# Performance work log

Hardware: AMD Instinct MI355X
Metric: run time of the kernel (lower is better)

Reference implementation:

```python
import jax, jax.numpy as jnp
import numpy as np

B, SEQ, PRED, DM = 16, 2048, 2048, 64
P = SEQ + PRED            # PointNum = 4096, per-node feature length
NLAYER, HID = 3, 4096     # MLPNums, ggdmodel hidden sizes
NH, HS = 16, 4096         # NumAttentionHeads, HiddenSize
G_CONST, K = 1.0, 8
NN = DM * DM              # 4096 == P, MHSA input dim (required by original code)


def setup_inputs() -> dict:
    key = jax.random.key(0)
    ks = jax.random.split(key, 11)
    s_mlp = 1.0 / np.sqrt(P).astype(np.float32)
    s_att = 1.0 / np.sqrt(NN).astype(np.float32)
    s_out = 1.0 / np.sqrt(HS).astype(np.float32)
    return {
        "x": jax.random.normal(ks[0], (B, P, DM), jnp.float32),
        "W_mlp": jax.random.normal(ks[1], (NLAYER, P, HID), jnp.float32) * s_mlp,
        "b_mlp": jnp.zeros((NLAYER, HID), jnp.float32),
        "Wq": jax.random.normal(ks[2], (NN, HS), jnp.float32) * s_att,
        "bq": jnp.zeros((HS,), jnp.float32),
        "Wk": jax.random.normal(ks[3], (NN, HS), jnp.float32) * s_att,
        "bk": jnp.zeros((HS,), jnp.float32),
        "Wv": jax.random.normal(ks[4], (NN, HS), jnp.float32) * s_att,
        "bv": jnp.zeros((HS,), jnp.float32),
        "Wo": jax.random.normal(ks[5], (HS, HS), jnp.float32) * s_out,
        "bo": jnp.zeros((HS,), jnp.float32),
    }


def _grav_adj(h):
    # h: [B, N, D] node features -> symmetrized, top-K masked gravity adjacency [B, N, N]
    norm = jnp.linalg.norm(h, axis=-1)                      # [B, N]
    m = jnp.sum(h, axis=-1) / norm                          # node "mass"
    sim = jnp.einsum('bnd,bmd->bnm', h, h) / (norm[:, :, None] * norm[:, None, :])
    F = G_CONST * m[:, :, None] * m[:, None, :] * sim * sim  # gravity matrix
    kth = jax.lax.top_k(F, K)[0][..., -1:]                  # per-row Kth largest value
    F = jnp.where(F >= kth, F, 0.0)                         # keep only top-K per row
    F = jnp.maximum(F, 0.0)                                 # ReLU
    return 0.5 * (F + jnp.swapaxes(F, -1, -2))              # symmetrize


def reference(x, W_mlp, b_mlp, Wq, bq, Wk, bk, Wv, bv, Wo, bo):
    h = jnp.swapaxes(x, 1, 2)                               # [B, N=DM, P]
    adjs = [_grav_adj(h)]
    for l in range(NLAYER):                                 # each MLP applied to the same h
        hv = h @ W_mlp[l] + b_mlp[l]                        # [B, N, HID]
        adjs.append(_grav_adj(hv))
    A = jnp.stack(adjs, axis=1)                             # [B, L, N, N], L = NLAYER + 1
    Lseq = A.shape[1]
    tok = A.reshape(B, Lseq, NN)                            # L tokens of dim N*N
    dh = HS // NH
    q = (tok @ Wq + bq).reshape(B, Lseq, NH, dh)
    k = (tok @ Wk + bk).reshape(B, Lseq, NH, dh)
    v = (tok @ Wv + bv).reshape(B, Lseq, NH, dh)
    scores = jnp.einsum('blhd,bmhd->bhlm', q, k) / np.sqrt(dh).astype(np.float32)
    attn = jax.nn.softmax(scores, axis=-1)
    ctx = jnp.einsum('bhlm,bmhd->blhd', attn, v).reshape(B, Lseq, HS)
    out = ctx @ Wo + bo                                     # [B, L, HS]
    return jnp.where(out > 0.5, out, 0.0)
```

## Files before the change

kernel.cpp:

```cpp
#include <hip/hip_runtime.h>
#include <math.h>


#define B16 16
#define PDIM 4096
#define NNODE 64
#define NCHUNK 32
#define KCG 128

typedef __attribute__((ext_vector_type(8))) short bf16x8;
typedef __attribute__((ext_vector_type(4))) float f32x4;
typedef __attribute__((ext_vector_type(4))) unsigned short us4;
typedef __attribute__((ext_vector_type(8))) unsigned short us8;

__device__ inline void split2(float x, unsigned short& h, unsigned short& l) {
  unsigned u = __float_as_uint(x);
  unsigned hu = (u + 0x7fffu + ((u >> 16) & 1u)) & 0xffff0000u;
  h = (unsigned short)(hu >> 16);
  float lo = x - __uint_as_float(hu);
  unsigned u2 = __float_as_uint(lo);
  l = (unsigned short)((u2 + 0x7fffu + ((u2 >> 16) & 1u)) >> 16);
}

__device__ inline void gload16(const void* g, void* lds) {
  __builtin_amdgcn_global_load_lds((const unsigned int*)g, (unsigned int*)lds, 16, 0, 0);
}

__global__ __launch_bounds__(256) void k_transpose(const float* __restrict__ x,
                                                   float* __restrict__ h,
                                                   unsigned short* __restrict__ AhT,
                                                   unsigned short* __restrict__ AlT,
                                                   int mode) {
  __shared__ float t[64][65];
  int b = blockIdx.y;
  int p0 = blockIdx.x * 64;
  const float* xb = x + (size_t)b * PDIM * NNODE;
#pragma unroll
  for (int i = 0; i < 16; ++i) {
    int e = i * 256 + threadIdx.x;
    int p = e >> 6, n = e & 63;
    t[p][n] = xb[(size_t)p0 * 64 + e];
  }
  __syncthreads();
  if (mode != 2) {
    float* hb = h + (size_t)b * NNODE * PDIM;
#pragma unroll
    for (int i = 0; i < 16; ++i) {
      int e = i * 256 + threadIdx.x;
      int n = e >> 6, p = e & 63;
      hb[(size_t)n * PDIM + p0 + p] = t[p][n];
    }
  }
  if (mode == 0) return;
#pragma unroll
  for (int j = 0; j < 2; ++j) {
    int cid = j * 256 + threadIdx.x;
    int n2 = cid >> 3, kg8 = cid & 7;
    us8 hv_, lv_;
#pragma unroll
    for (int e = 0; e < 8; ++e) {
      unsigned short hh, ll;
      split2(t[kg8 * 8 + e][n2], hh, ll);
      hv_[e] = hh; lv_[e] = ll;
    }
    int m = b * 64 + n2;
    int ks = (p0 >> 5) + (kg8 >> 2);
    size_t idx = (((size_t)(m >> 7) * 128 + ks) * 8 + ((m >> 4) & 7)) * 512 +
                 (size_t)((n2 & 15) + 16 * (kg8 & 3)) * 8;
    *(us8*)&AhT[idx] = hv_;
    *(us8*)&AlT[idx] = lv_;
  }
}

__global__ __launch_bounds__(256) void k_wsplit(const float* __restrict__ W,
                                                unsigned short* __restrict__ WhT,
                                                unsigned short* __restrict__ WlT) {
  __shared__ float Wt[32][132];
  int nb = blockIdx.x, kb = blockIdx.y;
  int tid = threadIdx.x;
#pragma unroll
  for (int i = 0; i < 4; ++i) {
    int idx = i * 256 + tid;
    int row = idx >> 5, c4 = idx & 31;
    float4 v = *(const float4*)&W[(size_t)(kb * 32 + row) * 4096 + nb * 128 + c4 * 4];
    *(float4*)&Wt[row][c4 * 4] = v;
  }
  __syncthreads();
#pragma unroll
  for (int j = 0; j < 2; ++j) {
    int cid = j * 256 + tid;
    int nl = cid & 127, kg = cid >> 7;
    us8 hv_, lv_;
#pragma unroll
    for (int e = 0; e < 8; ++e) {
      unsigned short hh, ll;
      split2(Wt[kg * 8 + e][nl], hh, ll);
      hv_[e] = hh; lv_[e] = ll;
    }
    size_t idx = (((size_t)nb * 128 + kb) * 8 + (nl >> 4)) * 512 +
                 (size_t)((nl & 15) + 16 * kg) * 8;
    *(us8*)&WhT[idx] = hv_;
    *(us8*)&WlT[idx] = lv_;
  }
}

__global__ __launch_bounds__(512) void k_gemm_bf16(
    const unsigned short* __restrict__ Ah, const unsigned short* __restrict__ Al,
    const unsigned short* __restrict__ Bh, const unsigned short* __restrict__ Bl,
    float* __restrict__ Cp, int Ksteps, int ksplit, int N, int mstore) {
  __shared__ unsigned short sAh[2][4096], sAl[2][4096];
  __shared__ unsigned short sBh[2][4096], sBl[2][4096];
  int tid = threadIdx.x;
  int l = tid & 63, wid = tid >> 6;
  int wr = wid >> 2, wc = wid & 3;
  int nb = blockIdx.x, mb = blockIdx.y, z = blockIdx.z;
  int spp = Ksteps / ksplit;
  int ks0 = z * spp;

  const size_t abase = ((size_t)mb * Ksteps + ks0) * 4096 + tid * 8;
  const size_t bbase = ((size_t)nb * Ksteps + ks0) * 4096 + tid * 8;

  f32x4 acc[4][2];
#pragma unroll
  for (int i = 0; i < 4; ++i)
#pragma unroll
    for (int j = 0; j < 2; ++j) acc[i][j] = (f32x4){0.f, 0.f, 0.f, 0.f};

  gload16(Ah + abase, &sAh[0][tid * 8]);
  gload16(Al + abase, &sAl[0][tid * 8]);
  gload16(Bh + bbase, &sBh[0][tid * 8]);
  gload16(Bl + bbase, &sBl[0][tid * 8]);
  gload16(Ah + abase + 4096, &sAh[1][tid * 8]);
  gload16(Al + abase + 4096, &sAl[1][tid * 8]);
  gload16(Bh + bbase + 4096, &sBh[1][tid * 8]);
  gload16(Bl + bbase + 4096, &sBl[1][tid * 8]);

  for (int t = 0; t < spp; ++t) {
    int buf = t & 1;
    if (t + 1 < spp) asm volatile("s_waitcnt vmcnt(4)" ::: "memory");
    else             asm volatile("s_waitcnt vmcnt(0)" ::: "memory");
    __builtin_amdgcn_s_barrier();
    asm volatile("" ::: "memory");

    bf16x8 ah[4], al4[4], bh2[2], bl2[2];
#pragma unroll
    for (int mt = 0; mt < 4; ++mt) {
      ah[mt]  = *(const bf16x8*)&sAh[buf][(wr * 4 + mt) * 512 + l * 8];
      al4[mt] = *(const bf16x8*)&sAl[buf][(wr * 4 + mt) * 512 + l * 8];
    }
#pragma unroll
    for (int nt = 0; nt < 2; ++nt) {
      bh2[nt] = *(const bf16x8*)&sBh[buf][(wc * 2 + nt) * 512 + l * 8];
      bl2[nt] = *(const bf16x8*)&sBl[buf][(wc * 2 + nt) * 512 + l * 8];
    }
#pragma unroll
    for (int mt = 0; mt < 4; ++mt)
#pragma unroll
      for (int nt = 0; nt < 2; ++nt) {
        acc[mt][nt] = __builtin_amdgcn_mfma_f32_16x16x32_bf16(ah[mt],  bh2[nt], acc[mt][nt], 0, 0, 0);
        acc[mt][nt] = __builtin_amdgcn_mfma_f32_16x16x32_bf16(ah[mt],  bl2[nt], acc[mt][nt], 0, 0, 0);
        acc[mt][nt] = __builtin_amdgcn_mfma_f32_16x16x32_bf16(al4[mt], bh2[nt], acc[mt][nt], 0, 0, 0);
      }

    asm volatile("" ::: "memory");
    __builtin_amdgcn_s_barrier();
    asm volatile("" ::: "memory");
    if (t + 2 < spp) {
      size_t off = (size_t)(t + 2) * 4096;
      gload16(Ah + abase + off, &sAh[buf][tid * 8]);
      gload16(Al + abase + off, &sAl[buf][tid * 8]);
      gload16(Bh + bbase + off, &sBh[buf][tid * 8]);
      gload16(Bl + bbase + off, &sBl[buf][tid * 8]);
    }
  }

  int n0 = nb * 128, m0 = mb * 128;
  float* Cz = Cp + (size_t)z * mstore * N;
#pragma unroll
  for (int mt = 0; mt < 4; ++mt)
#pragma unroll
    for (int nt = 0; nt < 2; ++nt) {
      int col = n0 + wc * 32 + nt * 16 + (l & 15);
#pragma unroll
      for (int r = 0; r < 4; ++r) {
        int row = m0 + wr * 64 + mt * 16 + ((l >> 4) << 2) + r;
        if (row < mstore) Cz[(size_t)row * N + col] = acc[mt][nt][r];
      }
    }
}

__global__ __launch_bounds__(512) void k_gemm_wsf32(
    const unsigned short* __restrict__ Ah, const unsigned short* __restrict__ Al,
    const float* __restrict__ W0, const float* __restrict__ W1,
    const float* __restrict__ W2, float* __restrict__ Cp, int ksplit) {
  __shared__ unsigned short sAh[2][2048], sAl[2][2048];
  __shared__ unsigned short sBh[2][4096], sBl[2][4096];
  int tid = threadIdx.x;
  int l = tid & 63, wid = tid >> 6;
  int wr = wid >> 2, wc = wid & 3;
  int nb = blockIdx.x, z = blockIdx.z;
  int mat = z / ksplit, kz = z - mat * ksplit;
  const float* W = (mat == 0) ? W0 : ((mat == 1) ? W1 : W2);
  int nsteps = 128 / ksplit;
  int ks0 = kz * nsteps;
  int n0 = nb * 128;

  const float* wbase = W + (size_t)((l >> 4) * 8) * 4096 + n0 + wid * 16 + (l & 15);
  int sidx = wid * 512 + l * 8;

  f32x4 acc[2][2];
#pragma unroll
  for (int i = 0; i < 2; ++i)
#pragma unroll
    for (int j = 0; j < 2; ++j) acc[i][j] = (f32x4){0.f, 0.f, 0.f, 0.f};

  {
    if (tid < 256) gload16(Ah + (size_t)ks0 * 4096 + tid * 8, &sAh[0][tid * 8]);
    else           gload16(Al + (size_t)ks0 * 4096 + (tid - 256) * 8, &sAl[0][(tid - 256) * 8]);
    float wv[8];
#pragma unroll
    for (int e = 0; e < 8; ++e) wv[e] = wbase[(size_t)ks0 * 131072 + (size_t)e * 4096];
    us8 hi, lo;
#pragma unroll
    for (int e = 0; e < 8; ++e) {
      unsigned short hh, ll;
      split2(wv[e], hh, ll);
      hi[e] = hh; lo[e] = ll;
    }
    *(us8*)&sBh[0][sidx] = hi;
    *(us8*)&sBl[0][sidx] = lo;
  }
  __syncthreads();

  int buf = 0;
  for (int t = 0; t < nsteps; ++t) {
    bool more = (t + 1 < nsteps);
    float wv[8];
    if (more) {
      int ks = ks0 + t + 1;
      if (tid < 256) gload16(Ah + (size_t)ks * 4096 + tid * 8, &sAh[buf ^ 1][tid * 8]);
      else           gload16(Al + (size_t)ks * 4096 + (tid - 256) * 8, &sAl[buf ^ 1][(tid - 256) * 8]);
#pragma unroll
      for (int e = 0; e < 8; ++e) wv[e] = wbase[(size_t)ks * 131072 + (size_t)e * 4096];
    }
    bf16x8 aH[2], aL[2], bH[2], bL[2];
#pragma unroll
    for (int i = 0; i < 2; ++i) {
      aH[i] = *(const bf16x8*)&sAh[buf][(wr * 2 + i) * 512 + l * 8];
      aL[i] = *(const bf16x8*)&sAl[buf][(wr * 2 + i) * 512 + l * 8];
      bH[i] = *(const bf16x8*)&sBh[buf][(wc * 2 + i) * 512 + l * 8];
      bL[i] = *(const bf16x8*)&sBl[buf][(wc * 2 + i) * 512 + l * 8];
    }
#pragma unroll
    for (int i = 0; i < 2; ++i)
#pragma unroll
      for (int j = 0; j < 2; ++j) {
        acc[i][j] = __builtin_amdgcn_mfma_f32_16x16x32_bf16(aH[i], bH[j], acc[i][j], 0, 0, 0);
        acc[i][j] = __builtin_amdgcn_mfma_f32_16x16x32_bf16(aH[i], bL[j], acc[i][j], 0, 0, 0);
        acc[i][j] = __builtin_amdgcn_mfma_f32_16x16x32_bf16(aL[i], bH[j], acc[i][j], 0, 0, 0);
      }
    if (more) {
      us8 hi, lo;
#pragma unroll
      for (int e = 0; e < 8; ++e) {
        unsigned short hh, ll;
        split2(wv[e], hh, ll);
        hi[e] = hh; lo[e] = ll;
      }
      *(us8*)&sBh[buf ^ 1][sidx] = hi;
      *(us8*)&sBl[buf ^ 1][sidx] = lo;
    }
    __syncthreads();
    buf ^= 1;
  }

  float* Cz = Cp + (size_t)z * 262144;
#pragma unroll
  for (int i = 0; i < 2; ++i)
#pragma unroll
    for (int j = 0; j < 2; ++j) {
      int col = n0 + wc * 32 + j * 16 + (l & 15);
#pragma unroll
      for (int r = 0; r < 4; ++r) {
        int row = (wr * 2 + i) * 16 + ((l >> 4) << 2) + r;
        Cz[(size_t)row * 4096 + col] = acc[i][j][r];
      }
    }
}

__global__ __launch_bounds__(256) void k_gram_fuse(
    const float* __restrict__ Cp, const float* __restrict__ bias,
    float* __restrict__ Gp, float* __restrict__ Sp, int nparts) {
  __shared__ unsigned short sZh[2048], sZl[2048];
  int zk = blockIdx.x, b = blockIdx.y;
  int tid = threadIdx.x;
  int l = tid & 63, w = tid >> 6;
  int srow = tid >> 2, skq = tid & 3;
  const float* cbase = Cp + (size_t)(b * 64 + srow) * 4096;
  int swidx = (srow >> 4) * 512 + (skq * 16 + (srow & 15)) * 8;

  f32x4 acc[4], racc;
#pragma unroll
  for (int j = 0; j < 4; ++j) acc[j] = (f32x4){0.f, 0.f, 0.f, 0.f};
  racc = (f32x4){0.f, 0.f, 0.f, 0.f};
  bf16x8 ones;
#pragma unroll
  for (int e = 0; e < 8; ++e) ones[e] = (short)0x3F80;

  for (int s = 0; s < 4; ++s) {
    int k0 = zk * 128 + s * 32 + skq * 8;
    float v[8];
#pragma unroll
    for (int e = 0; e < 8; ++e) v[e] = bias[k0 + e];
    for (int p = 0; p < nparts; ++p) {
      const float* pp = cbase + (size_t)p * 4194304 + k0;
      float4 a0 = *(const float4*)pp;
      float4 a1 = *(const float4*)(pp + 4);
      v[0] += a0.x; v[1] += a0.y; v[2] += a0.z; v[3] += a0.w;
      v[4] += a1.x; v[5] += a1.y; v[6] += a1.z; v[7] += a1.w;
    }
    us8 hi, lo;
#pragma unroll
    for (int e = 0; e < 8; ++e) {
      unsigned short hh, ll;
      split2(v[e], hh, ll);
      hi[e] = hh; lo[e] = ll;
    }
    *(us8*)&sZh[swidx] = hi;
    *(us8*)&sZl[swidx] = lo;
    __syncthreads();
    bf16x8 bh[4], bl4[4];
#pragma unroll
    for (int nt = 0; nt < 4; ++nt) {
      bh[nt]  = *(const bf16x8*)&sZh[nt * 512 + l * 8];
      bl4[nt] = *(const bf16x8*)&sZl[nt * 512 + l * 8];
    }
    bf16x8 ah = bh[w], al = bl4[w];
#pragma unroll
    for (int nt = 0; nt < 4; ++nt) {
      acc[nt] = __builtin_amdgcn_mfma_f32_16x16x32_bf16(ah, bh[nt], acc[nt], 0, 0, 0);
      acc[nt] = __builtin_amdgcn_mfma_f32_16x16x32_bf16(ah, bl4[nt], acc[nt], 0, 0, 0);
      acc[nt] = __builtin_amdgcn_mfma_f32_16x16x32_bf16(al, bh[nt], acc[nt], 0, 0, 0);
    }
    racc = __builtin_amdgcn_mfma_f32_16x16x32_bf16(ah, ones, racc, 0, 0, 0);
    racc = __builtin_amdgcn_mfma_f32_16x16x32_bf16(al, ones, racc, 0, 0, 0);
    __syncthreads();
  }

  float* Gz = Gp + ((size_t)zk * B16 + b) * 4096;
#pragma unroll
  for (int nt = 0; nt < 4; ++nt) {
    int col = nt * 16 + (l & 15);
#pragma unroll
    for (int r = 0; r < 4; ++r) {
      int row = w * 16 + ((l >> 4) << 2) + r;
      Gz[row * 64 + col] = acc[nt][r];
    }
  }
  if ((l & 15) == 0) {
    float* Sz = Sp + ((size_t)zk * B16 + b) * 64;
#pragma unroll
    for (int r = 0; r < 4; ++r) Sz[w * 16 + ((l >> 4) << 2) + r] = racc[r];
  }
}

__global__ __launch_bounds__(256) void k_gram_mfma(
    const unsigned short* __restrict__ Zh, const unsigned short* __restrict__ Zl,
    float* __restrict__ Gp, float* __restrict__ Sp,
    int bs1, int ks_stride, int nsteps) {
  __shared__ unsigned short sZh[2][2048], sZl[2][2048];
  int z = blockIdx.x, b = blockIdx.y;
  int tid = threadIdx.x;
  int l = tid & 63, w = tid >> 6;
  size_t zbase = (size_t)(b >> 1) * 524288 + (size_t)(b & 1) * bs1;
  int ks0 = z * nsteps;

  f32x4 acc[4], racc;
#pragma unroll
  for (int j = 0; j < 4; ++j) acc[j] = (f32x4){0.f, 0.f, 0.f, 0.f};
  racc = (f32x4){0.f, 0.f, 0.f, 0.f};
  bf16x8 ones;
#pragma unroll
  for (int e = 0; e < 8; ++e) ones[e] = (short)0x3F80;

  gload16(Zh + zbase + (size_t)ks0 * ks_stride + tid * 8, &sZh[0][tid * 8]);
  gload16(Zl + zbase + (size_t)ks0 * ks_stride + tid * 8, &sZl[0][tid * 8]);
  __syncthreads();

  int buf = 0;
  for (int t = 0; t < nsteps; ++t) {
    if (t + 1 < nsteps) {
      size_t off = zbase + (size_t)(ks0 + t + 1) * ks_stride + tid * 8;
      gload16(Zh + off, &sZh[buf ^ 1][tid * 8]);
      gload16(Zl + off, &sZl[buf ^ 1][tid * 8]);
    }
    bf16x8 bh[4], bl4[4];
#pragma unroll
    for (int nt = 0; nt < 4; ++nt) {
      bh[nt]  = *(const bf16x8*)&sZh[buf][nt * 512 + l * 8];
      bl4[nt] = *(const bf16x8*)&sZl[buf][nt * 512 + l * 8];
    }
    bf16x8 ah = bh[w], al = bl4[w];
#pragma unroll
    for (int nt = 0; nt < 4; ++nt) {
      acc[nt] = __builtin_amdgcn_mfma_f32_16x16x32_bf16(ah, bh[nt], acc[nt], 0, 0, 0);
      acc[nt] = __builtin_amdgcn_mfma_f32_16x16x32_bf16(ah, bl4[nt], acc[nt], 0, 0, 0);
      acc[nt] = __builtin_amdgcn_mfma_f32_16x16x32_bf16(al, bh[nt], acc[nt], 0, 0, 0);
    }
    racc = __builtin_amdgcn_mfma_f32_16x16x32_bf16(ah, ones, racc, 0, 0, 0);
    racc = __builtin_amdgcn_mfma_f32_16x16x32_bf16(al, ones, racc, 0, 0, 0);
    __syncthreads();
    buf ^= 1;
  }

  float* Gz = Gp + ((size_t)z * B16 + b) * 4096;
#pragma unroll
  for (int nt = 0; nt < 4; ++nt) {
    int col = nt * 16 + (l & 15);
#pragma unroll
    for (int r = 0; r < 4; ++r) {
      int row = w * 16 + ((l >> 4) << 2) + r;
      Gz[row * 64 + col] = acc[nt][r];
    }
  }
  if ((l & 15) == 0) {
    float* Sz = Sp + ((size_t)z * B16 + b) * 64;
#pragma unroll
    for (int r = 0; r < 4; ++r) Sz[w * 16 + ((l >> 4) << 2) + r] = racc[r];
  }
}

__global__ __launch_bounds__(256) void k_gred(const float* __restrict__ Gp,
                                              const float* __restrict__ Sp,
                                              float* __restrict__ G,
                                              float* __restrict__ S, int slot, int nc) {
  int idx = blockIdx.x * 256 + threadIdx.x;
  if (idx < 65536) {
    float s = 0.f;
    for (int c = 0; c < nc; ++c) s += Gp[(size_t)c * 65536 + idx];
    G[(size_t)slot * 65536 + idx] = s;
  } else if (idx < 66560) {
    int i2 = idx - 65536;
    float s = 0.f;
    for (int c = 0; c < nc; ++c) s += Sp[(size_t)c * 1024 + i2];
    S[(size_t)slot * 1024 + i2] = s;
  }
}

__global__ __launch_bounds__(256) void k_redqkv(const float* __restrict__ Cp,
                                                const float* __restrict__ bq,
                                                const float* __restrict__ bk,
                                                const float* __restrict__ bv,
                                                float* __restrict__ q,
                                                float* __restrict__ k,
                                                float* __restrict__ v) {
  int idx = blockIdx.x * 256 + threadIdx.x;
  int mat = idx >> 18;
  int rn = idx & ((1 << 18) - 1);
  int n = rn & 4095;
  const float* base = Cp + (size_t)mat * 16 * 262144;
  float s = 0.f;
#pragma unroll
  for (int p = 0; p < 16; ++p) s += base[(size_t)p * 262144 + rn];
  if (mat == 0) q[rn] = s + bq[n];
  else if (mat == 1) k[rn] = s + bk[n];
  else v[rn] = s + bv[n];
}

__global__ __launch_bounds__(256) void k_redN(const float* __restrict__ Cp,
                                              const float* __restrict__ bias,
                                              float* __restrict__ dst,
                                              int nparts, int thr) {
  int idx = blockIdx.x * 256 + threadIdx.x;
  float s = bias[idx & 4095];
  for (int p = 0; p < nparts; ++p) s += Cp[(size_t)p * 262144 + idx];
  if (thr) s = (s > 0.5f) ? s : 0.f;
  dst[idx] = s;
}

__device__ inline float wmax64(float v) {
#pragma unroll
  for (int off = 32; off; off >>= 1) v = fmaxf(v, __shfl_xor(v, off));
  return v;
}

__global__ __launch_bounds__(256) void k_adj_t(const float* __restrict__ G,
                                               const float* __restrict__ S,
                                               unsigned short* __restrict__ tokh,
                                               unsigned short* __restrict__ tokl) {
  __shared__ float Fm[64][64];
  __shared__ float nrm[64], mm[64];
  int b = blockIdx.x >> 2, lz = blockIdx.x & 3;
  int tid = threadIdx.x;
  int j = tid & 63, w = tid >> 6;
  const float* Gb = G + ((size_t)lz * B16 + b) * 4096;
  const float* Sb = S + ((size_t)lz * B16 + b) * 64;
  if (tid < 64) {
    float nj = sqrtf(Gb[tid * 64 + tid]);
    nrm[tid] = nj;
    mm[tid] = Sb[tid] / nj;
  }
  __syncthreads();
  for (int i = w; i < 64; i += 4) {
    float g = Gb[i * 64 + j];
    float sim = g / (nrm[i] * nrm[j]);
    Fm[i][j] = mm[i] * mm[j] * sim * sim;
  }
  __syncthreads();
  for (int i = w; i < 64; i += 4) {
    float f = Fm[i][j];
    int cnt = 0;
#pragma unroll
    for (int u4 = 0; u4 < 16; ++u4) {
      float4 q = *(const float4*)&Fm[i][u4 * 4];
      cnt += (q.x > f) + (q.y > f) + (q.z > f) + (q.w > f);
    }
    float cand = (cnt <= 7) ? f : INFINITY;
#pragma unroll
    for (int off = 32; off; off >>= 1) cand = fminf(cand, __shfl_xor(cand, off));
    float fm = (f >= cand) ? fmaxf(f, 0.f) : 0.f;
    Fm[i][j] = fm;
  }
  __syncthreads();
  int r = b * 4 + lz;
  int mt = r >> 4, rl = r & 15;
#pragma unroll
  for (int c = 0; c < 2; ++c) {
    int cid = tid * 2 + c;
    int jj0 = cid >> 3, g = cid & 7;
    us8 hv_, lv_;
#pragma unroll
    for (int e = 0; e < 8; ++e) {
      int kcol = g * 8 + e;
      float val = 0.5f * (Fm[jj0][kcol] + Fm[kcol][jj0]);
      unsigned short hh, ll;
      split2(val, hh, ll);
      hv_[e] = hh; lv_[e] = ll;
    }
    int ks = jj0 * 2 + (g >> 2);
    size_t idx = ((size_t)ks * 8 + mt) * 512 + (size_t)(rl + 16 * (g & 3)) * 8;
    *(us8*)&tokh[idx] = hv_;
    *(us8*)&tokl[idx] = lv_;
  }
}

__global__ __launch_bounds__(64) void k_attn_t(const float* __restrict__ q,
                                               const float* __restrict__ k,
                                               const float* __restrict__ v,
                                               unsigned short* __restrict__ ctxh,
                                               unsigned short* __restrict__ ctxl) {
  __shared__ float cb[4][256];
  int hd = blockIdx.x, b = blockIdx.y;
  int t = threadIdx.x;
  float qr[4][4], kr[4][4], vr[4][4];
#pragma unroll
  for (int l = 0; l < 4; ++l)
#pragma unroll
    for (int s = 0; s < 4; ++s) {
      size_t off = ((size_t)(b * 4 + l)) * 4096 + hd * 256 + t + s * 64;
      qr[l][s] = q[off]; kr[l][s] = k[off]; vr[l][s] = v[off];
    }
  float sc[4][4];
#pragma unroll
  for (int l = 0; l < 4; ++l)
#pragma unroll
    for (int m = 0; m < 4; ++m) {
      float p = 0.f;
#pragma unroll
      for (int s = 0; s < 4; ++s) p = fmaf(qr[l][s], kr[m][s], p);
#pragma unroll
      for (int off = 32; off; off >>= 1) p += __shfl_xor(p, off);
      sc[l][m] = p * (1.0f / 16.0f);
    }
  float at[4][4];
#pragma unroll
  for (int l = 0; l < 4; ++l) {
    float mx = fmaxf(fmaxf(sc[l][0], sc[l][1]), fmaxf(sc[l][2], sc[l][3]));
    float e0 = expf(sc[l][0] - mx), e1 = expf(sc[l][1] - mx);
    float e2 = expf(sc[l][2] - mx), e3 = expf(sc[l][3] - mx);
    float d = e0 + e1 + e2 + e3;
    at[l][0] = e0 / d; at[l][1] = e1 / d; at[l][2] = e2 / d; at[l][3] = e3 / d;
  }
#pragma unroll
  for (int l = 0; l < 4; ++l)
#pragma unroll
    for (int s = 0; s < 4; ++s) {
      float c = 0.f;
#pragma unroll
      for (int m = 0; m < 4; ++m) c = fmaf(at[l][m], vr[m][s], c);
      cb[l][s * 64 + t] = c;
    }
  __syncthreads();
  int lq = t >> 4, c16 = t & 15;
  int mt = b >> 2, rl = (b & 3) * 4 + lq;
#pragma unroll
  for (int e8 = 0; e8 < 2; ++e8) {
    us8 hv_, lv_;
#pragma unroll
    for (int e = 0; e < 8; ++e) {
      unsigned short hh, ll;
      split2(cb[lq][c16 * 16 + e8 * 8 + e], hh, ll);
      hv_[e] = hh; lv_[e] = ll;
    }
    int ks = hd * 8 + (c16 >> 1);
    size_t idx = ((size_t)ks * 8 + mt) * 512 + (size_t)(rl + 16 * ((c16 * 2 + e8) & 3)) * 8;
    *(us8*)&ctxh[idx] = hv_;
    *(us8*)&ctxl[idx] = lv_;
  }
}

__global__ __launch_bounds__(256) void k_gram_partial(const float* __restrict__ Z,
                                                      float* __restrict__ Gp,
                                                      float* __restrict__ Sp) {
  __shared__ float Zt[KCG][68];
  int c = blockIdx.x, b = blockIdx.y;
  int tid = threadIdx.x;
  const float* Zb = Z + (size_t)b * NNODE * PDIM + c * KCG;
#pragma unroll
  for (int i = 0; i < 32; ++i) {
    int e = i * 256 + tid;
    int r = e >> 7, kk = e & 127;
    Zt[kk][r] = Zb[(size_t)r * PDIM + kk];
  }
  __syncthreads();
  int ii = tid >> 2, j0 = (tid & 3) << 4;
  float acc[16] = {};
  for (int kk = 0; kk < KCG; ++kk) {
    float zi = Zt[kk][ii];
    float4 z0 = *(const float4*)&Zt[kk][j0 + 0];
    float4 z1 = *(const float4*)&Zt[kk][j0 + 4];
    float4 z2 = *(const float4*)&Zt[kk][j0 + 8];
    float4 z3 = *(const float4*)&Zt[kk][j0 + 12];
    acc[0] = fmaf(zi, z0.x, acc[0]);   acc[1] = fmaf(zi, z0.y, acc[1]);
    acc[2] = fmaf(zi, z0.z, acc[2]);   acc[3] = fmaf(zi, z0.w, acc[3]);
    acc[4] = fmaf(zi, z1.x, acc[4]);   acc[5] = fmaf(zi, z1.y, acc[5]);
    acc[6] = fmaf(zi, z1.z, acc[6]);   acc[7] = fmaf(zi, z1.w, acc[7]);
    acc[8] = fmaf(zi, z2.x, acc[8]);   acc[9] = fmaf(zi, z2.y, acc[9]);
    acc[10] = fmaf(zi, z2.z, acc[10]); acc[11] = fmaf(zi, z2.w, acc[11]);
    acc[12] = fmaf(zi, z3.x, acc[12]); acc[13] = fmaf(zi, z3.y, acc[13]);
    acc[14] = fmaf(zi, z3.z, acc[14]); acc[15] = fmaf(zi, z3.w, acc[15]);
  }
  float* gp = Gp + ((size_t)c * B16 + b) * 4096 + ii * 64 + j0;
#pragma unroll
  for (int j = 0; j < 16; ++j) gp[j] = acc[j];
  if (tid < 64) {
    float s = 0.f;
    for (int kk = 0; kk < KCG; ++kk) s += Zt[kk][tid];
    Sp[((size_t)c * B16 + b) * 64 + tid] = s;
  }
}

__global__ __launch_bounds__(256) void k_gram_reduce(const float* __restrict__ Gp,
                                                     const float* __restrict__ Sp,
                                                     float* __restrict__ G,
                                                     float* __restrict__ S, int slot) {
  int idx = blockIdx.x * 256 + threadIdx.x;
  if (idx < B16 * 4096) {
    float s = 0.f;
    for (int c = 0; c < NCHUNK; ++c) s += Gp[(size_t)c * (B16 * 4096) + idx];
    G[(size_t)slot * (B16 * 4096) + idx] = s;
  } else {
    int idx2 = idx - B16 * 4096;
    float s = 0.f;
    for (int c = 0; c < NCHUNK; ++c) s += Sp[(size_t)c * (B16 * 64) + idx2];
    S[(size_t)slot * (B16 * 64) + idx2] = s;
  }
}

__global__ __launch_bounds__(256) void k_gemm_mfma(
    const float* __restrict__ A, const float* __restrict__ B0,
    const float* __restrict__ B1, const float* __restrict__ B2,
    const float* __restrict__ bias, float* __restrict__ C,
    int mrows, int mstore, int N, int K, int ksplit) {
  __shared__ __align__(16) unsigned short sA[2][8][64][8];
  __shared__ __align__(16) unsigned short sB[2][8][64][8];
  int z = blockIdx.z;
  int mat = z / ksplit, ks = z - mat * ksplit;
  const float* Bm = (mat == 0) ? B0 : ((mat == 1) ? B1 : B2);
  int kchunk = K / ksplit;
  int k0 = ks * kchunk, k1 = k0 + kchunk;
  int tid = threadIdx.x;
  int l = tid & 63;
  int wr = (tid >> 7) & 1, wc = (tid >> 6) & 1;
  int m0 = blockIdx.y * 128, n0g = blockIdx.x * 128;
  bool activeM = (m0 + wr * 64) < mstore;
  int am = tid >> 1;
  int arow = m0 + am; if (arow >= mrows) arow = mrows - 1;
  const float* Arow = A + (size_t)arow * K;
  int amt = am >> 4;
  int bk = tid >> 3;
  int bnb = (tid & 7) * 4;
  int bg = bk >> 3, bslot = bk & 7;
  f32x4 acc[4][4];
#pragma unroll
  for (int i = 0; i < 4; ++i)
#pragma unroll
    for (int j = 0; j < 4; ++j) acc[i][j] = (f32x4){0.f, 0.f, 0.f, 0.f};
  for (int kb = k0; kb < k1; kb += 32) {
    __syncthreads();
#pragma unroll
    for (int i = 0; i < 4; ++i) {
      int kq = (tid & 1) * 4 + i * 8;
      float4 a = *(const float4*)(Arow + kb + kq);
      unsigned short h0, h1, h2, h3, l0, l1, l2, l3;
      split2(a.x, h0, l0); split2(a.y, h1, l1);
      split2(a.z, h2, l2); split2(a.w, h3, l3);
      int lane_t = (am & 15) + 16 * (kq >> 3);
      int sb = kq & 4;
      *(us4*)&sA[0][amt][lane_t][sb] = (us4){h0, h1, h2, h3};
      *(us4*)&sA[1][amt][lane_t][sb] = (us4){l0, l1, l2, l3};
    }
    {
      const float* Brow = Bm + (size_t)(kb + bk) * N + n0g;
#pragma unroll
      for (int i = 0; i < 4; ++i) {
        int n = bnb + i * 32;
        int nt = n >> 4, nr = n & 15;
        float4 b = *(const float4*)(Brow + n);
        float be[4] = {b.x, b.y, b.z, b.w};
#pragma unroll
        for (int e = 0; e < 4; ++e) {
          unsigned short hh, ll;
          split2(be[e], hh, ll);
          sB[0][nt][nr + e + 16 * bg][bslot] = hh;
          sB[1][nt][nr + e + 16 * bg][bslot] = ll;
        }
      }
    }
    __syncthreads();
    if (!activeM) continue;
    bf16x8 ah[4], al[4], bh[4], bl[4];
#pragma unroll
    for (int t = 0; t < 4; ++t) {
      ah[t] = *(const bf16x8*)&sA[0][wr * 4 + t][l][0];
      al[t] = *(const bf16x8*)&sA[1][wr * 4 + t][l][0];
      bh[t] = *(const bf16x8*)&sB[0][wc * 4 + t][l][0];
      bl[t] = *(const bf16x8*)&sB[1][wc * 4 + t][l][0];
    }
#pragma unroll
    for (int mt = 0; mt < 4; ++mt)
#pragma unroll
      for (int nt = 0; nt < 4; ++nt) {
        acc[mt][nt] = __builtin_amdgcn_mfma_f32_16x16x32_bf16(ah[mt], bh[nt], acc[mt][nt], 0, 0, 0);
        acc[mt][nt] = __builtin_amdgcn_mfma_f32_16x16x32_bf16(ah[mt], bl[nt], acc[mt][nt], 0, 0, 0);
        acc[mt][nt] = __builtin_amdgcn_mfma_f32_16x16x32_bf16(al[mt], bh[nt], acc[mt][nt], 0, 0, 0);
      }
  }
  if (!activeM) return;
  float* Cz = C + (size_t)z * mstore * N;
#pragma unroll
  for (int mt = 0; mt < 4; ++mt)
#pragma unroll
    for (int nt = 0; nt < 4; ++nt) {
      int col = n0g + wc * 64 + nt * 16 + (l & 15);
      float badd = bias ? bias[col] : 0.f;
#pragma unroll
      for (int r = 0; r < 4; ++r) {
        int row = m0 + wr * 64 + mt * 16 + ((l >> 4) << 2) + r;
        if (row < mstore) Cz[(size_t)row * N + col] = acc[mt][nt][r] + badd;
      }
    }
}

__global__ __launch_bounds__(64) void k_adj_fb(const float* __restrict__ G,
                                               const float* __restrict__ S,
                                               float* __restrict__ tok) {
  __shared__ float Fm[64][64];
  __shared__ float nrm[64], mm[64];
  int b = blockIdx.x >> 2, lz = blockIdx.x & 3;
  int j = threadIdx.x;
  const float* Gb = G + ((size_t)lz * B16 + b) * 4096;
  const float* Sb = S + ((size_t)lz * B16 + b) * 64;
  float nj = sqrtf(Gb[j * 64 + j]);
  nrm[j] = nj;
  mm[j] = Sb[j] / nj;
  __syncthreads();
  for (int i = 0; i < 64; ++i) {
    float g = Gb[i * 64 + j];
    float sim = g / (nrm[i] * nj);
    float F = mm[i] * mm[j] * sim * sim;
    float v = F;
    bool act = true;
    float kth = 0.f;
#pragma unroll
    for (int it = 0; it < 8; ++it) {
      float mv = wmax64(act ? v : -INFINITY);
      kth = mv;
      unsigned long long ball = __ballot(act && (v == mv));
      int first = __ffsll(ball) - 1;
      if (j == first) act = false;
    }
    float fm = (F >= kth) ? F : 0.f;
    Fm[i][j] = fmaxf(fm, 0.f);
  }
  __syncthreads();
  float* tb = tok + ((size_t)b * 4 + lz) * 4096;
  for (int i = 0; i < 64; ++i) tb[i * 64 + j] = 0.5f * (Fm[i][j] + Fm[j][i]);
}

__global__ __launch_bounds__(256) void k_qkv_reduce(const float* __restrict__ Cp,
                                                    const float* __restrict__ bq,
                                                    const float* __restrict__ bk,
                                                    const float* __restrict__ bv,
                                                    float* __restrict__ q,
                                                    float* __restrict__ k,
                                                    float* __restrict__ v) {
  int idx = blockIdx.x * 256 + threadIdx.x;
  int mat = idx >> 18;
  int rn = idx & ((1 << 18) - 1);
  int n = rn & 4095;
  const float* base = Cp + (size_t)mat * 4 * 262144;
  float s = base[rn] + base[rn + 262144] + base[rn + 2 * 262144] + base[rn + 3 * 262144];
  if (mat == 0) q[rn] = s + bq[n];
  else if (mat == 1) k[rn] = s + bk[n];
  else v[rn] = s + bv[n];
}

__global__ __launch_bounds__(64) void k_attn_fb(const float* __restrict__ q,
                                                const float* __restrict__ k,
                                                const float* __restrict__ v,
                                                float* __restrict__ ctx) {
  int hd = blockIdx.x, b = blockIdx.y;
  int t = threadIdx.x;
  float qr[4][4], kr[4][4], vr[4][4];
#pragma unroll
  for (int l = 0; l < 4; ++l)
#pragma unroll
    for (int s = 0; s < 4; ++s) {
      size_t off = ((size_t)(b * 4 + l)) * 4096 + hd * 256 + t + s * 64;
      qr[l][s] = q[off]; kr[l][s] = k[off]; vr[l][s] = v[off];
    }
  float sc[4][4];
#pragma unroll
  for (int l = 0; l < 4; ++l)
#pragma unroll
    for (int m = 0; m < 4; ++m) {
      float p = 0.f;
#pragma unroll
      for (int s = 0; s < 4; ++s) p = fmaf(qr[l][s], kr[m][s], p);
#pragma unroll
      for (int off = 32; off; off >>= 1) p += __shfl_xor(p, off);
      sc[l][m] = p * (1.0f / 16.0f);
    }
  float at[4][4];
#pragma unroll
  for (int l = 0; l < 4; ++l) {
    float mx = fmaxf(fmaxf(sc[l][0], sc[l][1]), fmaxf(sc[l][2], sc[l][3]));
    float e0 = expf(sc[l][0] - mx), e1 = expf(sc[l][1] - mx);
    float e2 = expf(sc[l][2] - mx), e3 = expf(sc[l][3] - mx);
    float d = e0 + e1 + e2 + e3;
    at[l][0] = e0 / d; at[l][1] = e1 / d; at[l][2] = e2 / d; at[l][3] = e3 / d;
  }
#pragma unroll
  for (int l = 0; l < 4; ++l)
#pragma unroll
    for (int s = 0; s < 4; ++s) {
      float c = 0.f;
#pragma unroll
      for (int m = 0; m < 4; ++m) c = fmaf(at[l][m], vr[m][s], c);
      ctx[((size_t)(b * 4 + l)) * 4096 + hd * 256 + t + s * 64] = c;
    }
}

__global__ __launch_bounds__(256) void k_out_reduce(const float* __restrict__ Cp,
                                                    const float* __restrict__ bo,
                                                    float* __restrict__ out) {
  int idx = blockIdx.x * 256 + threadIdx.x;
  int n = idx & 4095;
  float s = bo[n];
#pragma unroll
  for (int p = 0; p < 8; ++p) s += Cp[(size_t)p * 262144 + idx];
  out[idx] = (s > 0.5f) ? s : 0.f;
}

extern "C" void kernel_launch(void* const* d_in, const int* in_sizes, int n_in,
                              void* d_out, int out_size, void* d_ws, size_t ws_size,
                              hipStream_t stream) {
  const float* x     = (const float*)d_in[0];
  const float* W_mlp = (const float*)d_in[1];
  const float* b_mlp = (const float*)d_in[2];
  const float* Wq = (const float*)d_in[3]; const float* bq = (const float*)d_in[4];
  const float* Wk = (const float*)d_in[5]; const float* bk = (const float*)d_in[6];
  const float* Wv = (const float*)d_in[7]; const float* bv = (const float*)d_in[8];
  const float* Wo = (const float*)d_in[9]; const float* bo = (const float*)d_in[10];
  float* out = (float*)d_out;
  float* ws = (float*)d_ws;

  float* h   = ws;
  float* Gp  = ws + 8388608;
  float* Sp  = ws + 10485760;
  float* G   = ws + 10518528;
  float* S   = ws + 10780672;

  const size_t NEED = 50368512ull * 4ull;
  if (ws_size >= NEED) {
    float* q   = ws + 10784768;
    float* kk  = ws + 11046912;
    float* vv  = ws + 11309056;
    unsigned short* AhT = (unsigned short*)(ws + 11571200);
    unsigned short* AlT = (unsigned short*)(ws + 13668352);
    unsigned short* WhT = (unsigned short*)(ws + 15765504);
    unsigned short* WlT = (unsigned short*)(ws + 24154112);
    float* Cp           = ws + 32542720;
    unsigned short* tokh = (unsigned short*)(ws + 49319936);
    unsigned short* tokl = (unsigned short*)(ws + 49582080);
    unsigned short* ctxh = (unsigned short*)(ws + 49844224);
    unsigned short* ctxl = (unsigned short*)(ws + 50106368);

    k_transpose<<<dim3(64, 16), 256, 0, stream>>>(x, h, AhT, AlT, 2);

    k_gram_mfma<<<dim3(8, 16), 256, 0, stream>>>(AhT, AlT, Gp, Sp, 2048, 4096, 16);
    k_gred<<<260, 256, 0, stream>>>(Gp, Sp, G, S, 0, 8);

    for (int l = 0; l < 3; ++l) {
      k_wsplit<<<dim3(32, 128), 256, 0, stream>>>(W_mlp + (size_t)l * 16777216, WhT, WlT);
      k_gemm_bf16<<<dim3(32, 8, 2), 512, 0, stream>>>(AhT, AlT, WhT, WlT, Cp,
                                                      128, 2, 4096, 1024);
      k_gram_fuse<<<dim3(32, 16), 256, 0, stream>>>(Cp, b_mlp + (size_t)l * 4096,
                                                    Gp, Sp, 2);
      k_gred<<<260, 256, 0, stream>>>(Gp, Sp, G, S, l + 1, 32);
    }

    k_adj_t<<<64, 256, 0, stream>>>(G, S, tokh, tokl);

    k_gemm_wsf32<<<dim3(32, 1, 48), 512, 0, stream>>>(tokh, tokl, Wq, Wk, Wv, Cp, 16);
    k_redqkv<<<3072, 256, 0, stream>>>(Cp, bq, bk, bv, q, kk, vv);

    k_attn_t<<<dim3(16, 16), 64, 0, stream>>>(q, kk, vv, ctxh, ctxl);

    k_gemm_wsf32<<<dim3(32, 1, 16), 512, 0, stream>>>(ctxh, ctxl, Wo, Wo, Wo, Cp, 16);
    k_redN<<<1024, 256, 0, stream>>>(Cp, bo, out, 16, 1);
  } else {
    float* hv  = ws + 4194304;
    float* tok = ws + 10784768;
    float* q   = ws + 11046912;
    float* kk  = ws + 11309056;
    float* vv  = ws + 11571200;
    float* ctx = ws + 11833344;
    float* qkvp = hv;
    float* op   = h;

    k_transpose<<<dim3(64, 16), 256, 0, stream>>>(x, h, (unsigned short*)0,
                                                  (unsigned short*)0, 0);
    k_gram_partial<<<dim3(NCHUNK, 16), 256, 0, stream>>>(h, Gp, Sp);
    k_gram_reduce<<<260, 256, 0, stream>>>(Gp, Sp, G, S, 0);
    for (int l = 0; l < 3; ++l) {
      const float* Wl = W_mlp + (size_t)l * PDIM * 4096;
      const float* bl = b_mlp + (size_t)l * 4096;
      k_gemm_mfma<<<dim3(32, 8, 1), 256, 0, stream>>>(h, Wl, Wl, Wl, bl, hv,
                                                      1024, 1024, 4096, 4096, 1);
      k_gram_partial<<<dim3(NCHUNK, 16), 256, 0, stream>>>(hv, Gp, Sp);
      k_gram_reduce<<<260, 256, 0, stream>>>(Gp, Sp, G, S, l + 1);
    }
    k_adj_fb<<<64, 64, 0, stream>>>(G, S, tok);
    k_gemm_mfma<<<dim3(32, 1, 12), 256, 0, stream>>>(tok, Wq, Wk, Wv, nullptr, qkvp,
                                                     64, 64, 4096, 4096, 4);
    k_qkv_reduce<<<3072, 256, 0, stream>>>(qkvp, bq, bk, bv, q, kk, vv);
    k_attn_fb<<<dim3(16, 16), 64, 0, stream>>>(q, kk, vv, ctx);
    k_gemm_mfma<<<dim3(32, 1, 8), 256, 0, stream>>>(ctx, Wo, Wo, Wo, nullptr, op,
                                                    64, 64, 4096, 4096, 8);
    k_out_reduce<<<1024, 256, 0, stream>>>(op, bo, out);
  }
}
```

Before: 557.8 us.

## Split split-bf16 GEMM step into three phases with staggered prefetch

Restructures the inner loop of the split-bf16 GEMM into three MFMA phases (hi*hi, hi*lo, lo*hi). Each phase is followed by a barrier and reissues the global-to-LDS prefetch for whichever buffer is now free, so the next stage's loads start earlier and overlap with the remaining MFMAs. The change also adds s_setprio around the MFMA groups and sched_barriers to pin the instruction order. In exchange each step now has more barriers, and the correctness of the vmcnt(4) wait relies on the reordered load issue order.

New measurement: 570.0 us. +2.2%, slower.

```diff
diff --git a/kernel.cpp b/kernel.cpp
--- a/kernel.cpp
+++ b/kernel.cpp
@@ -127,51 +127,75 @@
     for (int j = 0; j < 2; ++j) acc[i][j] = (f32x4){0.f, 0.f, 0.f, 0.f};
 
   gload16(Ah + abase, &sAh[0][tid * 8]);
-  gload16(Al + abase, &sAl[0][tid * 8]);
   gload16(Bh + bbase, &sBh[0][tid * 8]);
   gload16(Bl + bbase, &sBl[0][tid * 8]);
+  gload16(Al + abase, &sAl[0][tid * 8]);
   gload16(Ah + abase + 4096, &sAh[1][tid * 8]);
-  gload16(Al + abase + 4096, &sAl[1][tid * 8]);
   gload16(Bh + bbase + 4096, &sBh[1][tid * 8]);
   gload16(Bl + bbase + 4096, &sBl[1][tid * 8]);
+  gload16(Al + abase + 4096, &sAl[1][tid * 8]);
 
   for (int t = 0; t < spp; ++t) {
     int buf = t & 1;
+    bool pf = (t + 2 < spp);
+    size_t off2 = (size_t)(t + 2) * 4096;
+
     if (t + 1 < spp) asm volatile("s_waitcnt vmcnt(4)" ::: "memory");
     else             asm volatile("s_waitcnt vmcnt(0)" ::: "memory");
     __builtin_amdgcn_s_barrier();
-    asm volatile("" ::: "memory");
+    __builtin_amdgcn_sched_barrier(0);
 
     bf16x8 ah[4], al4[4], bh2[2], bl2[2];
 #pragma unroll
-    for (int mt = 0; mt < 4; ++mt) {
-      ah[mt]  = *(const bf16x8*)&sAh[buf][(wr * 4 + mt) * 512 + l * 8];
-      al4[mt] = *(const bf16x8*)&sAl[buf][(wr * 4 + mt) * 512 + l * 8];
-    }
-#pragma unroll
-    for (int nt = 0; nt < 2; ++nt) {
+    for (int mt = 0; mt < 4; ++mt)
+      ah[mt] = *(const bf16x8*)&sAh[buf][(wr * 4 + mt) * 512 + l * 8];
+#pragma unroll
+    for (int nt = 0; nt < 2; ++nt)
       bh2[nt] = *(const bf16x8*)&sBh[buf][(wc * 2 + nt) * 512 + l * 8];
-      bl2[nt] = *(const bf16x8*)&sBl[buf][(wc * 2 + nt) * 512 + l * 8];
-    }
+    __builtin_amdgcn_s_setprio(1);
 #pragma unroll
     for (int mt = 0; mt < 4; ++mt)
 #pragma unroll
-      for (int nt = 0; nt < 2; ++nt) {
-        acc[mt][nt] = __builtin_amdgcn_mfma_f32_16x16x32_bf16(ah[mt],  bh2[nt], acc[mt][nt], 0, 0, 0);
-        acc[mt][nt] = __builtin_amdgcn_mfma_f32_16x16x32_bf16(ah[mt],  bl2[nt], acc[mt][nt], 0, 0, 0);
-        acc[mt][nt] = __builtin_amdgcn_mfma_f32_16x16x32_bf16(al4[mt], bh2[nt], acc[mt][nt], 0, 0, 0);
-      }
-
+      for (int nt = 0; nt < 2; ++nt)
+        acc[mt][nt] = __builtin_amdgcn_mfma_f32_16x16x32_bf16(ah[mt], bh2[nt], acc[mt][nt], 0, 0, 0);
+    __builtin_amdgcn_s_setprio(0);
     asm volatile("" ::: "memory");
     __builtin_amdgcn_s_barrier();
+    __builtin_amdgcn_sched_barrier(0);
+
+    if (pf) {
+      gload16(Ah + abase + off2, &sAh[buf][tid * 8]);
+      gload16(Bh + bbase + off2, &sBh[buf][tid * 8]);
+    }
+#pragma unroll
+    for (int nt = 0; nt < 2; ++nt)
+      bl2[nt] = *(const bf16x8*)&sBl[buf][(wc * 2 + nt) * 512 + l * 8];
+    __builtin_amdgcn_s_setprio(1);
+#pragma unroll
+    for (int mt = 0; mt < 4; ++mt)
+#pragma unroll
+      for (int nt = 0; nt < 2; ++nt)
+        acc[mt][nt] = __builtin_amdgcn_mfma_f32_16x16x32_bf16(ah[mt], bl2[nt], acc[mt][nt], 0, 0, 0);
+    __builtin_amdgcn_s_setprio(0);
     asm volatile("" ::: "memory");
-    if (t + 2 < spp) {
-      size_t off = (size_t)(t + 2) * 4096;
-      gload16(Ah + abase + off, &sAh[buf][tid * 8]);
-      gload16(Al + abase + off, &sAl[buf][tid * 8]);
-      gload16(Bh + bbase + off, &sBh[buf][tid * 8]);
-      gload16(Bl + bbase + off, &sBl[buf][tid * 8]);
-    }
+    __builtin_amdgcn_s_barrier();
+    __builtin_amdgcn_sched_barrier(0);
+
+    if (pf) gload16(Bl + bbase + off2, &sBl[buf][tid * 8]);
+#pragma unroll
+    for (int mt = 0; mt < 4; ++mt)
+      al4[mt] = *(const bf16x8*)&sAl[buf][(wr * 4 + mt) * 512 + l * 8];
+    __builtin_amdgcn_s_setprio(1);
+#pragma unroll
+    for (int mt = 0; mt < 4; ++mt)
+#pragma unroll
+      for (int nt = 0; nt < 2; ++nt)
+        acc[mt][nt] = __builtin_amdgcn_mfma_f32_16x16x32_bf16(al4[mt], bh2[nt], acc[mt][nt], 0, 0, 0);
+    __builtin_amdgcn_s_setprio(0);
+    asm volatile("" ::: "memory");
+    __builtin_amdgcn_s_barrier();
+    __builtin_amdgcn_sched_barrier(0);
+    if (pf) gload16(Al + abase + off2, &sAl[buf][tid * 8]);
   }
 
   int n0 = nb * 128, m0 = mb * 128;
```

## Load bf16 GEMM fragments directly from global memory, dropping LDS staging

Applied to the files above, without the earlier changes.

Removes the double-buffered LDS staging, the barriers and the async global-to-LDS prefetch in the split-bf16 GEMM kernel. Each wave now reads its MFMA fragments straight from the pre-swizzled global layout. This saves LDS traffic and synchronisation, but each A fragment is now read by all four column waves and each B fragment by both row waves from global/L2 with no reuse, and there is no software prefetch to hide latency.

New measurement: 797.6 us. 1.43x slower.

```diff
diff --git a/kernel.cpp b/kernel.cpp
--- a/kernel.cpp
+++ b/kernel.cpp
@@ -108,8 +108,6 @@
     const unsigned short* __restrict__ Ah, const unsigned short* __restrict__ Al,
     const unsigned short* __restrict__ Bh, const unsigned short* __restrict__ Bl,
     float* __restrict__ Cp, int Ksteps, int ksplit, int N, int mstore) {
-  __shared__ unsigned short sAh[2][4096], sAl[2][4096];
-  __shared__ unsigned short sBh[2][4096], sBl[2][4096];
   int tid = threadIdx.x;
   int l = tid & 63, wid = tid >> 6;
   int wr = wid >> 2, wc = wid & 3;
@@ -117,8 +115,8 @@
   int spp = Ksteps / ksplit;
   int ks0 = z * spp;
 
-  const size_t abase = ((size_t)mb * Ksteps + ks0) * 4096 + tid * 8;
-  const size_t bbase = ((size_t)nb * Ksteps + ks0) * 4096 + tid * 8;
+  size_t abase = ((size_t)mb * Ksteps + ks0) * 4096 + (size_t)(wr * 4) * 512 + l * 8;
+  size_t bbase = ((size_t)nb * Ksteps + ks0) * 4096 + (size_t)(wc * 2) * 512 + l * 8;
 
   f32x4 acc[4][2];
 #pragma unroll
@@ -126,32 +124,19 @@
 #pragma unroll
     for (int j = 0; j < 2; ++j) acc[i][j] = (f32x4){0.f, 0.f, 0.f, 0.f};
 
-  gload16(Ah + abase, &sAh[0][tid * 8]);
-  gload16(Al + abase, &sAl[0][tid * 8]);
-  gload16(Bh + bbase, &sBh[0][tid * 8]);
-  gload16(Bl + bbase, &sBl[0][tid * 8]);
-  gload16(Ah + abase + 4096, &sAh[1][tid * 8]);
-  gload16(Al + abase + 4096, &sAl[1][tid * 8]);
-  gload16(Bh + bbase + 4096, &sBh[1][tid * 8]);
-  gload16(Bl + bbase + 4096, &sBl[1][tid * 8]);
-
   for (int t = 0; t < spp; ++t) {
-    int buf = t & 1;
-    if (t + 1 < spp) asm volatile("s_waitcnt vmcnt(4)" ::: "memory");
-    else             asm volatile("s_waitcnt vmcnt(0)" ::: "memory");
-    __builtin_amdgcn_s_barrier();
-    asm volatile("" ::: "memory");
-
+    size_t ao = abase + (size_t)t * 4096;
+    size_t bo = bbase + (size_t)t * 4096;
     bf16x8 ah[4], al4[4], bh2[2], bl2[2];
 #pragma unroll
     for (int mt = 0; mt < 4; ++mt) {
-      ah[mt]  = *(const bf16x8*)&sAh[buf][(wr * 4 + mt) * 512 + l * 8];
-      al4[mt] = *(const bf16x8*)&sAl[buf][(wr * 4 + mt) * 512 + l * 8];
+      ah[mt]  = *(const bf16x8*)(Ah + ao + mt * 512);
+      al4[mt] = *(const bf16x8*)(Al + ao + mt * 512);
     }
 #pragma unroll
     for (int nt = 0; nt < 2; ++nt) {
-      bh2[nt] = *(const bf16x8*)&sBh[buf][(wc * 2 + nt) * 512 + l * 8];
-      bl2[nt] = *(const bf16x8*)&sBl[buf][(wc * 2 + nt) * 512 + l * 8];
+      bh2[nt] = *(const bf16x8*)(Bh + bo + nt * 512);
+      bl2[nt] = *(const bf16x8*)(Bl + bo + nt * 512);
     }
 #pragma unroll
     for (int mt = 0; mt < 4; ++mt)
@@ -161,17 +146,6 @@
         acc[mt][nt] = __builtin_amdgcn_mfma_f32_16x16x32_bf16(ah[mt],  bl2[nt], acc[mt][nt], 0, 0, 0);
         acc[mt][nt] = __builtin_amdgcn_mfma_f32_16x16x32_bf16(al4[mt], bh2[nt], acc[mt][nt], 0, 0, 0);
       }
-
-    asm volatile("" ::: "memory");
-    __builtin_amdgcn_s_barrier();
-    asm volatile("" ::: "memory");
-    if (t + 2 < spp) {
-      size_t off = (size_t)(t + 2) * 4096;
-      gload16(Ah + abase + off, &sAh[buf][tid * 8]);
-      gload16(Al + abase + off, &sAl[buf][tid * 8]);
-      gload16(Bh + bbase + off, &sBh[buf][tid * 8]);
-      gload16(Bl + bbase + off, &sBl[buf][tid * 8]);
-    }
   }
 
   int n0 = nb * 128, m0 = mb * 128;
```
